# Kernel optimization log

Hardware: AMD Instinct MI355X
Metric: run time of the kernel (lower is better)

The kernel has to match this reference:

```python
import jax, jax.numpy as jnp
import numpy as np

B, S, D, H = 2, 2048, 1024, 16
DK = D // H


def setup_inputs() -> dict:
    key = jax.random.key(0)
    ks = jax.random.split(key, 7)
    return {
        "query": jax.random.normal(ks[0], (B, S, D), jnp.float32),
        "key": jax.random.normal(ks[1], (B, S, D), jnp.float32),
        "value": jax.random.normal(ks[2], (B, S, D), jnp.float32),
        "w_q": jax.random.normal(ks[3], (D, D), jnp.float32) * (1.0 / np.sqrt(D)),
        "w_k": jax.random.normal(ks[4], (D, D), jnp.float32) * (1.0 / np.sqrt(D)),
        "w_v": jax.random.normal(ks[5], (D, D), jnp.float32) * (1.0 / np.sqrt(D)),
        "w_o": jax.random.normal(ks[6], (D, D), jnp.float32) * (1.0 / np.sqrt(D)),
    }


def reference(query, key, value, w_q, w_k, w_v, w_o):
    # Linear(bias=False) in torch computes x @ W.T where W is [out, in].
    Q = jnp.einsum('bsd,ed->bse', query, w_q)
    K = jnp.einsum('bsd,ed->bse', key, w_k)
    V = jnp.einsum('bsd,ed->bse', value, w_v)
    # split heads: [B, H, S, DK]
    Q = Q.reshape(B, S, H, DK).transpose(0, 2, 1, 3)
    K = K.reshape(B, S, H, DK).transpose(0, 2, 1, 3)
    V = V.reshape(B, S, H, DK).transpose(0, 2, 1, 3)
    scale = 1.0 / np.sqrt(DK).astype(np.float32)
    scores = jnp.einsum('bhqd,bhkd->bhqk', Q, K) * scale  # [B,H,S,S]
    attn = jax.nn.softmax(scores, axis=-1)
    context = jnp.einsum('bhqk,bhkd->bhqd', attn, V)
    context = context.transpose(0, 2, 1, 3).reshape(B, S, D)
    return jnp.einsum('bsd,ed->bse', context, w_o)
```

## Files before the change

### kernel.cpp

```cpp
#include <hip/hip_runtime.h>

typedef unsigned short u16;
typedef unsigned int u32;
typedef __bf16 bf16x8 __attribute__((ext_vector_type(8)));
typedef float f32x4 __attribute__((ext_vector_type(4)));
typedef short s16x4 __attribute__((ext_vector_type(4)));

#define AS1 __attribute__((address_space(1)))
#define AS3 __attribute__((address_space(3)))

__device__ __forceinline__ f32x4 mfma16(bf16x8 a, bf16x8 b, f32x4 c) {
    return __builtin_amdgcn_mfma_f32_16x16x32_bf16(a, b, c, 0, 0, 0);
}
__device__ __forceinline__ f32x4 mfma16k16(s16x4 a, s16x4 b, f32x4 c) {
    return __builtin_amdgcn_mfma_f32_16x16x16bf16_1k(a, b, c, 0, 0, 0);
}

__device__ __forceinline__ u16 f2bf(float f) {
    return __builtin_bit_cast(u16, (__bf16)f);
}

__device__ __forceinline__ void gld16(const u16* g, u16* l) {
    __builtin_amdgcn_global_load_lds((AS1 void*)g, (AS3 void*)l, 16, 0, 0);
}

__device__ __forceinline__ void barrier_nodrain() {
    asm volatile("s_waitcnt lgkmcnt(0)" ::: "memory");
    __builtin_amdgcn_s_barrier();
    asm volatile("" ::: "memory");
}

__global__ __launch_bounds__(256) void cvt_all(const float* __restrict__ q, const float* __restrict__ k,
                                               const float* __restrict__ v, const float* __restrict__ wq,
                                               const float* __restrict__ wk, const float* __restrict__ wv,
                                               const float* __restrict__ wo, u16* __restrict__ qo,
                                               u16* __restrict__ ko, u16* __restrict__ vo,
                                               u16* __restrict__ wqo, u16* __restrict__ wko,
                                               u16* __restrict__ wvo, u16* __restrict__ woo) {
    const int y = blockIdx.y;
    const float* x; u16* o; int n;
    switch (y) {
        case 0: x = q; o = qo; n = 4 << 20; break;
        case 1: x = k; o = ko; n = 4 << 20; break;
        case 2: x = v; o = vo; n = 4 << 20; break;
        case 3: x = wq; o = wqo; n = 1 << 20; break;
        case 4: x = wk; o = wko; n = 1 << 20; break;
        case 5: x = wv; o = wvo; n = 1 << 20; break;
        default: x = wo; o = woo; n = 1 << 20; break;
    }
    int i = (blockIdx.x * 256 + threadIdx.x) * 4;
    if (i >= n) return;
    float4 vv = *(const float4*)(x + i);
    u32 lo = (u32)f2bf(vv.x) | ((u32)f2bf(vv.y) << 16);
    u32 hi = (u32)f2bf(vv.z) | ((u32)f2bf(vv.w) << 16);
    *(uint2*)(o + i) = make_uint2(lo, hi);
}

template <int BM, int BN, bool BF16OUT>
__device__ __forceinline__ void gemm_core(const u16* __restrict__ A, const u16* __restrict__ Bt,
                                          void* __restrict__ Cp, int K, int N, int m0, int n0,
                                          float oscale) {
    constexpr int WROWS = BM / 64;
    constexpr int WCOLS = 4 / WROWS;
    constexpr int BFR = BN / WCOLS / 16;
    __shared__ __align__(16) u16 As[BM * 32];
    __shared__ __align__(16) u16 Bs[BN * 32];
    const int tid = threadIdx.x;
    const int lane = tid & 63, wave = tid >> 6;
    const int l16 = lane & 15, q4 = lane >> 4;
    const int wm = (wave / WCOLS) * 64, wn = (wave % WCOLS) * (BFR * 16);

    const f32x4 fz = {0.f, 0.f, 0.f, 0.f};
    f32x4 acc[4][BFR];
#pragma unroll
    for (int i = 0; i < 4; ++i)
#pragma unroll
        for (int j = 0; j < BFR; ++j) acc[i][j] = fz;

    const int rseg = lane >> 2;
    const int ck = ((lane & 3) ^ ((lane >> 3) & 3)) * 8;
    const u16* Ag = A + (size_t)(m0 + wave * 16 + rseg) * K + ck;
    const u16* Bg = Bt + (size_t)(n0 + wave * 16 + rseg) * K + ck;

    const int swz = (q4 ^ ((l16 & 7) >> 1)) * 8;

    for (int k0 = 0; k0 < K; k0 += 32) {
        __syncthreads();
#pragma unroll
        for (int p = 0; p < BM / 64; ++p)
            gld16(Ag + (size_t)p * 64 * K + k0, As + p * 2048 + wave * 512);
#pragma unroll
        for (int p = 0; p < BN / 64; ++p)
            gld16(Bg + (size_t)p * 64 * K + k0, Bs + p * 2048 + wave * 512);
        __syncthreads();
        bf16x8 af[4], bfr[BFR];
#pragma unroll
        for (int i = 0; i < 4; ++i)
            af[i] = *(const bf16x8*)&As[(wm + i * 16 + l16) * 32 + swz];
#pragma unroll
        for (int j = 0; j < BFR; ++j)
            bfr[j] = *(const bf16x8*)&Bs[(wn + j * 16 + l16) * 32 + swz];
#pragma unroll
        for (int i = 0; i < 4; ++i)
#pragma unroll
            for (int j = 0; j < BFR; ++j) acc[i][j] = mfma16(af[i], bfr[j], acc[i][j]);
    }

#pragma unroll
    for (int i = 0; i < 4; ++i) {
        const int row = m0 + wm + i * 16 + q4 * 4;
#pragma unroll
        for (int j = 0; j < BFR; ++j) {
            const int col = n0 + wn + j * 16 + l16;
#pragma unroll
            for (int r = 0; r < 4; ++r) {
                const float vr = acc[i][j][r] * oscale;
                if constexpr (BF16OUT)
                    ((u16*)Cp)[(size_t)(row + r) * N + col] = f2bf(vr);
                else
                    ((float*)Cp)[(size_t)(row + r) * N + col] = vr;
            }
        }
    }
}

__global__ __launch_bounds__(256) void gemm_qkv(const u16* __restrict__ qb, const u16* __restrict__ kb,
                                                const u16* __restrict__ vb, const u16* __restrict__ wqb,
                                                const u16* __restrict__ wkb, const u16* __restrict__ wvb,
                                                u16* __restrict__ Qp, u16* __restrict__ Kp,
                                                u16* __restrict__ VtAll) {
    const int z = blockIdx.y;
    int x = blockIdx.x;
    if (z != 2) x = (x & 7) * 32 + (x >> 3);
    const u16 *A, *Bt;
    u16* C;
    int N, m0, n0;
    float sc = 1.0f;
    if (z == 0) {
        A = qb; Bt = wqb; C = Qp; N = 1024; m0 = (x >> 3) * 128; n0 = (x & 7) * 128;
        sc = 0.18033688011112042f;
    } else if (z == 1) {
        A = kb; Bt = wkb; C = Kp; N = 1024; m0 = (x >> 3) * 128; n0 = (x & 7) * 128;
    } else {
        A = wvb; Bt = vb; C = VtAll; N = 4096; m0 = (x >> 5) * 128; n0 = (x & 31) * 128;
    }
    gemm_core<128, 128, true>(A, Bt, C, 1024, N, m0, n0, sc);
}

__global__ __launch_bounds__(256) void gemm_out(const u16* __restrict__ ctx,
                                                const u16* __restrict__ wob,
                                                float* __restrict__ out) {
    const int xo = (blockIdx.x & 7) * 64 + (blockIdx.x >> 3);
    gemm_core<64, 128, false>(ctx, wob, out, 1024, 1024, (xo >> 3) * 64, (xo & 7) * 128, 1.0f);
}

__global__ __launch_bounds__(512, 4) void flash_attn(const u16* __restrict__ Qp,
                                                     const u16* __restrict__ Kp,
                                                     const u16* __restrict__ VtAll,
                                                     u16* __restrict__ Ctx) {
    constexpr int D = 1024, SS = 2048, LD = 72;
    __shared__ __align__(16) u16 Ks[2][64 * LD];
    __shared__ __align__(16) u16 Vts[2][64 * LD];

    const int tid = threadIdx.x;
    const int lane = tid & 63, wave = tid >> 6;
    const int l16 = lane & 15, q4 = lane >> 4;

    const int nb = blockIdx.x;
    const int orig = (nb & 7) * 64 + (nb >> 3);
    const int h = (orig >> 4) & 15, b = orig >> 8;
    const int q0 = (orig & 15) * 128 + wave * 16;

    bf16x8 qf[2];
    {
        const u16* Qb = Qp + (size_t)(b * SS + q0 + l16) * D + h * 64;
        qf[0] = *(const bf16x8*)(Qb + q4 * 8);
        qf[1] = *(const bf16x8*)(Qb + 32 + q4 * 8);
    }

    const f32x4 fz = {0.f, 0.f, 0.f, 0.f};
    f32x4 ot[4], lacc = fz;
#pragma unroll
    for (int dt = 0; dt < 4; ++dt) ot[dt] = fz;

    s16x4 onesA;
    onesA[0] = onesA[1] = onesA[2] = onesA[3] = (short)0x3F80;

    const int sr = tid >> 3;
    const int scol = (tid & 7) * 8;
    const int vswap = (sr >> 3) & 1;
    const int swV = (l16 >> 3) & 1;
    const u16* Kg = Kp + (size_t)(b * SS + sr) * D + h * 64 + scol;
    const u16* Vg = VtAll + (size_t)(h * 64 + sr) * 4096 + b * SS + scol;

    uint4 kv, vv;
    auto prefetch = [&](int kt) {
        kv = *(const uint4*)(Kg + (size_t)kt * D);
        vv = *(const uint4*)(Vg + kt);
    };
    auto stage = [&](int buf) {
        uint4 w = vswap ? make_uint4(vv.z, vv.w, vv.x, vv.y) : vv;
        *(uint4*)&Ks[buf][sr * LD + scol] = kv;
        *(uint4*)&Vts[buf][sr * LD + scol] = w;
    };

    prefetch(0);
    for (int kt = 0; kt < SS; kt += 64) {
        const int buf = (kt >> 6) & 1;
        stage(buf);
        const int nk = (kt + 64 < SS) ? kt + 64 : 0;
        prefetch(nk);
        barrier_nodrain();

        f32x4 st[4];
        __builtin_amdgcn_s_setprio(1);
#pragma unroll
        for (int nt = 0; nt < 4; ++nt) {
            const bf16x8 ka = *(const bf16x8*)&Ks[buf][(nt * 16 + l16) * LD + q4 * 8];
            const bf16x8 kb2 = *(const bf16x8*)&Ks[buf][(nt * 16 + l16) * LD + 32 + q4 * 8];
            f32x4 s = mfma16(ka, qf[0], fz);
            st[nt] = mfma16(kb2, qf[1], s);
        }
        __builtin_amdgcn_s_setprio(0);

        s16x4 p[4];
#pragma unroll
        for (int nt = 0; nt < 4; ++nt) {
#pragma unroll
            for (int r = 0; r < 4; ++r)
                p[nt][r] = (short)f2bf(__builtin_amdgcn_exp2f(st[nt][r]));
        }

        __builtin_amdgcn_s_setprio(1);
#pragma unroll
        for (int nt = 0; nt < 4; ++nt) {
#pragma unroll
            for (int dt = 0; dt < 4; ++dt) {
                const s16x4 va =
                    *(const s16x4*)&Vts[buf][(dt * 16 + l16) * LD + ((nt * 4 + q4) ^ swV) * 4];
                ot[dt] = mfma16k16(va, p[nt], ot[dt]);
            }
            lacc = mfma16k16(onesA, p[nt], lacc);
        }
        __builtin_amdgcn_s_setprio(0);
    }

    {
        const float inv = 1.f / lacc[0];
        u16* Cb = Ctx + (size_t)(b * SS + q0 + l16) * D + h * 64 + q4 * 4;
#pragma unroll
        for (int dt = 0; dt < 4; ++dt) {
            s16x4 w;
#pragma unroll
            for (int r = 0; r < 4; ++r) w[r] = (short)f2bf(ot[dt][r] * inv);
            *(s16x4*)(Cb + dt * 16) = w;
        }
    }
}

extern "C" void kernel_launch(void* const* d_in, const int* in_sizes, int n_in,
                              void* d_out, int out_size, void* d_ws, size_t ws_size,
                              hipStream_t stream) {
    const float* query = (const float*)d_in[0];
    const float* key   = (const float*)d_in[1];
    const float* value = (const float*)d_in[2];
    const float* w_q   = (const float*)d_in[3];
    const float* w_k   = (const float*)d_in[4];
    const float* w_v   = (const float*)d_in[5];
    const float* w_o   = (const float*)d_in[6];
    float* out = (float*)d_out;

    const size_t MEG = 1024 * 1024;
    if (ws_size < 64 * MEG) return;
    u16* ws = (u16*)d_ws;
    u16* qb    = ws;
    u16* kb    = ws + 4 * MEG;
    u16* vb    = ws + 8 * MEG;
    u16* wqb   = ws + 12 * MEG;
    u16* wkb   = ws + 13 * MEG;
    u16* wvb   = ws + 14 * MEG;
    u16* wob   = ws + 15 * MEG;
    u16* Qp    = ws + 16 * MEG;
    u16* Kp    = ws + 20 * MEG;
    u16* VtAll = ws + 24 * MEG;
    u16* ctx   = ws + 28 * MEG;

    cvt_all<<<dim3(4096, 7), 256, 0, stream>>>(query, key, value, w_q, w_k, w_v, w_o,
                                               qb, kb, vb, wqb, wkb, wvb, wob);
    gemm_qkv<<<dim3(256, 3), 256, 0, stream>>>(qb, kb, vb, wqb, wkb, wvb, Qp, Kp, VtAll);
    flash_attn<<<dim3(512), 512, 0, stream>>>(Qp, Kp, VtAll, ctx);
    gemm_out<<<dim3(512), 256, 0, stream>>>(ctx, wob, out);
}
```

Measured before the change: 214.2 us.

## Fuse fp32-to-bf16 conversion into GEMM loads with register prefetch

Removes the separate conversion kernel. The QKV and output GEMMs now read fp32 inputs and weights directly, convert them to bf16 in registers and write the result to LDS. The next k-tile is prefetched into registers to hide global latency. This saves a full read and write pass over the bf16 copies and one kernel launch. In exchange, each GEMM tile reads twice as many bytes from global memory (fp32 instead of bf16), uses more registers, and gives up the async global-to-LDS load path.

Result: slower. 241.7 us (+12.8%).

```diff
diff --git a/kernel.cpp b/kernel.cpp
--- a/kernel.cpp
+++ b/kernel.cpp
@@ -24,45 +24,27 @@
     __builtin_amdgcn_global_load_lds((AS1 void*)g, (AS3 void*)l, 16, 0, 0);
 }
 
+__device__ __forceinline__ uint4 pack8(float4 a, float4 b) {
+    return make_uint4((u32)f2bf(a.x) | ((u32)f2bf(a.y) << 16),
+                      (u32)f2bf(a.z) | ((u32)f2bf(a.w) << 16),
+                      (u32)f2bf(b.x) | ((u32)f2bf(b.y) << 16),
+                      (u32)f2bf(b.z) | ((u32)f2bf(b.w) << 16));
+}
+
 __device__ __forceinline__ void barrier_nodrain() {
     asm volatile("s_waitcnt lgkmcnt(0)" ::: "memory");
     __builtin_amdgcn_s_barrier();
     asm volatile("" ::: "memory");
 }
 
-__global__ __launch_bounds__(256) void cvt_all(const float* __restrict__ q, const float* __restrict__ k,
-                                               const float* __restrict__ v, const float* __restrict__ wq,
-                                               const float* __restrict__ wk, const float* __restrict__ wv,
-                                               const float* __restrict__ wo, u16* __restrict__ qo,
-                                               u16* __restrict__ ko, u16* __restrict__ vo,
-                                               u16* __restrict__ wqo, u16* __restrict__ wko,
-                                               u16* __restrict__ wvo, u16* __restrict__ woo) {
-    const int y = blockIdx.y;
-    const float* x; u16* o; int n;
-    switch (y) {
-        case 0: x = q; o = qo; n = 4 << 20; break;
-        case 1: x = k; o = ko; n = 4 << 20; break;
-        case 2: x = v; o = vo; n = 4 << 20; break;
-        case 3: x = wq; o = wqo; n = 1 << 20; break;
-        case 4: x = wk; o = wko; n = 1 << 20; break;
-        case 5: x = wv; o = wvo; n = 1 << 20; break;
-        default: x = wo; o = woo; n = 1 << 20; break;
-    }
-    int i = (blockIdx.x * 256 + threadIdx.x) * 4;
-    if (i >= n) return;
-    float4 vv = *(const float4*)(x + i);
-    u32 lo = (u32)f2bf(vv.x) | ((u32)f2bf(vv.y) << 16);
-    u32 hi = (u32)f2bf(vv.z) | ((u32)f2bf(vv.w) << 16);
-    *(uint2*)(o + i) = make_uint2(lo, hi);
-}
-
-template <int BM, int BN, bool BF16OUT>
-__device__ __forceinline__ void gemm_core(const u16* __restrict__ A, const u16* __restrict__ Bt,
+template <int BM, int BN, bool BF16OUT, bool AF32, bool BF32>
+__device__ __forceinline__ void gemm_core(const void* __restrict__ Apv, const void* __restrict__ Btv,
                                           void* __restrict__ Cp, int K, int N, int m0, int n0,
                                           float oscale) {
     constexpr int WROWS = BM / 64;
     constexpr int WCOLS = 4 / WROWS;
     constexpr int BFR = BN / WCOLS / 16;
+    constexpr int PA = BM / 64, PB = BN / 64;
     __shared__ __align__(16) u16 As[BM * 32];
     __shared__ __align__(16) u16 Bs[BN * 32];
     const int tid = threadIdx.x;
@@ -79,20 +61,57 @@
 
     const int rseg = lane >> 2;
     const int ck = ((lane & 3) ^ ((lane >> 3) & 3)) * 8;
-    const u16* Ag = A + (size_t)(m0 + wave * 16 + rseg) * K + ck;
-    const u16* Bg = Bt + (size_t)(n0 + wave * 16 + rseg) * K + ck;
+    const size_t arow = (size_t)(m0 + wave * 16 + rseg) * K + ck;
+    const size_t brow = (size_t)(n0 + wave * 16 + rseg) * K + ck;
+    const u16* Ag = (const u16*)Apv + arow;
+    const float* Af = (const float*)Apv + arow;
+    const u16* Bg = (const u16*)Btv + brow;
+    const float* Bf = (const float*)Btv + brow;
 
     const int swz = (q4 ^ ((l16 & 7) >> 1)) * 8;
+
+    float4 pfa[PA][2], pfb[PB][2];
+    auto prefetch = [&](int k0) {
+        if constexpr (AF32) {
+#pragma unroll
+            for (int p = 0; p < PA; ++p) {
+                pfa[p][0] = *(const float4*)(Af + (size_t)p * 64 * K + k0);
+                pfa[p][1] = *(const float4*)(Af + (size_t)p * 64 * K + k0 + 4);
+            }
+        }
+        if constexpr (BF32) {
+#pragma unroll
+            for (int p = 0; p < PB; ++p) {
+                pfb[p][0] = *(const float4*)(Bf + (size_t)p * 64 * K + k0);
+                pfb[p][1] = *(const float4*)(Bf + (size_t)p * 64 * K + k0 + 4);
+            }
+        }
+    };
+    prefetch(0);
 
     for (int k0 = 0; k0 < K; k0 += 32) {
         __syncthreads();
-#pragma unroll
-        for (int p = 0; p < BM / 64; ++p)
-            gld16(Ag + (size_t)p * 64 * K + k0, As + p * 2048 + wave * 512);
-#pragma unroll
-        for (int p = 0; p < BN / 64; ++p)
-            gld16(Bg + (size_t)p * 64 * K + k0, Bs + p * 2048 + wave * 512);
+        if constexpr (AF32) {
+#pragma unroll
+            for (int p = 0; p < PA; ++p)
+                *(uint4*)&As[p * 2048 + wave * 512 + lane * 8] = pack8(pfa[p][0], pfa[p][1]);
+        } else {
+#pragma unroll
+            for (int p = 0; p < PA; ++p)
+                gld16(Ag + (size_t)p * 64 * K + k0, As + p * 2048 + wave * 512);
+        }
+        if constexpr (BF32) {
+#pragma unroll
+            for (int p = 0; p < PB; ++p)
+                *(uint4*)&Bs[p * 2048 + wave * 512 + lane * 8] = pack8(pfb[p][0], pfb[p][1]);
+        } else {
+#pragma unroll
+            for (int p = 0; p < PB; ++p)
+                gld16(Bg + (size_t)p * 64 * K + k0, Bs + p * 2048 + wave * 512);
+        }
         __syncthreads();
+        if (k0 + 32 < K) prefetch(k0 + 32);
+
         bf16x8 af[4], bfr[BFR];
 #pragma unroll
         for (int i = 0; i < 4; ++i)
@@ -124,34 +143,34 @@
     }
 }
 
-__global__ __launch_bounds__(256) void gemm_qkv(const u16* __restrict__ qb, const u16* __restrict__ kb,
-                                                const u16* __restrict__ vb, const u16* __restrict__ wqb,
-                                                const u16* __restrict__ wkb, const u16* __restrict__ wvb,
+__global__ __launch_bounds__(256) void gemm_qkv(const float* __restrict__ q, const float* __restrict__ k,
+                                                const float* __restrict__ v, const float* __restrict__ wq,
+                                                const float* __restrict__ wk, const float* __restrict__ wv,
                                                 u16* __restrict__ Qp, u16* __restrict__ Kp,
                                                 u16* __restrict__ VtAll) {
     const int z = blockIdx.y;
     int x = blockIdx.x;
     if (z != 2) x = (x & 7) * 32 + (x >> 3);
-    const u16 *A, *Bt;
+    const float *A, *Bt;
     u16* C;
     int N, m0, n0;
     float sc = 1.0f;
     if (z == 0) {
-        A = qb; Bt = wqb; C = Qp; N = 1024; m0 = (x >> 3) * 128; n0 = (x & 7) * 128;
+        A = q; Bt = wq; C = Qp; N = 1024; m0 = (x >> 3) * 128; n0 = (x & 7) * 128;
         sc = 0.18033688011112042f;
     } else if (z == 1) {
-        A = kb; Bt = wkb; C = Kp; N = 1024; m0 = (x >> 3) * 128; n0 = (x & 7) * 128;
+        A = k; Bt = wk; C = Kp; N = 1024; m0 = (x >> 3) * 128; n0 = (x & 7) * 128;
     } else {
-        A = wvb; Bt = vb; C = VtAll; N = 4096; m0 = (x >> 5) * 128; n0 = (x & 31) * 128;
-    }
-    gemm_core<128, 128, true>(A, Bt, C, 1024, N, m0, n0, sc);
+        A = wv; Bt = v; C = VtAll; N = 4096; m0 = (x >> 5) * 128; n0 = (x & 31) * 128;
+    }
+    gemm_core<128, 128, true, true, true>(A, Bt, C, 1024, N, m0, n0, sc);
 }
 
 __global__ __launch_bounds__(256) void gemm_out(const u16* __restrict__ ctx,
-                                                const u16* __restrict__ wob,
+                                                const float* __restrict__ wo,
                                                 float* __restrict__ out) {
     const int xo = (blockIdx.x & 7) * 64 + (blockIdx.x >> 3);
-    gemm_core<64, 128, false>(ctx, wob, out, 1024, 1024, (xo >> 3) * 64, (xo & 7) * 128, 1.0f);
+    gemm_core<64, 128, false, false, true>(ctx, wo, out, 1024, 1024, (xo >> 3) * 64, (xo & 7) * 128, 1.0f);
 }
 
 __global__ __launch_bounds__(512, 4) void flash_attn(const u16* __restrict__ Qp,
@@ -271,23 +290,14 @@
     float* out = (float*)d_out;
 
     const size_t MEG = 1024 * 1024;
-    if (ws_size < 64 * MEG) return;
+    if (ws_size < 32 * MEG) return;
     u16* ws = (u16*)d_ws;
-    u16* qb    = ws;
-    u16* kb    = ws + 4 * MEG;
-    u16* vb    = ws + 8 * MEG;
-    u16* wqb   = ws + 12 * MEG;
-    u16* wkb   = ws + 13 * MEG;
-    u16* wvb   = ws + 14 * MEG;
-    u16* wob   = ws + 15 * MEG;
-    u16* Qp    = ws + 16 * MEG;
-    u16* Kp    = ws + 20 * MEG;
-    u16* VtAll = ws + 24 * MEG;
-    u16* ctx   = ws + 28 * MEG;
-
-    cvt_all<<<dim3(4096, 7), 256, 0, stream>>>(query, key, value, w_q, w_k, w_v, w_o,
-                                               qb, kb, vb, wqb, wkb, wvb, wob);
-    gemm_qkv<<<dim3(256, 3), 256, 0, stream>>>(qb, kb, vb, wqb, wkb, wvb, Qp, Kp, VtAll);
+    u16* Qp    = ws;
+    u16* Kp    = ws + 4 * MEG;
+    u16* VtAll = ws + 8 * MEG;
+    u16* ctx   = ws + 12 * MEG;
+
+    gemm_qkv<<<dim3(256, 3), 256, 0, stream>>>(query, key, value, w_q, w_k, w_v, Qp, Kp, VtAll);
     flash_attn<<<dim3(512), 512, 0, stream>>>(Qp, Kp, VtAll, ctx);
-    gemm_out<<<dim3(512), 256, 0, stream>>>(ctx, wob, out);
-}
+    gemm_out<<<dim3(512), 256, 0, stream>>>(ctx, w_o, out);
+}
```
